# Kernel optimization log

Hardware: AMD Instinct MI355X
Metric: run time of the kernel (lower is better)

The kernel has to match this reference:

```python
import jax, jax.numpy as jnp
import numpy as np

N_HEAD = 16
ROT_DIM = 64  # head_dim * rotary_percentage(1.0)
ROPE_BASE = 10000.0
NEG_INF = -1.0e9


def _rope_cos_sin(seq_len, rd):
    # freqs: [S, rd//2]; original code builds cos/sin per pair; we repeat each
    # entry twice so it applies to the interleaved (even, odd) pair layout.
    inv_freq = 1.0 / (ROPE_BASE ** (jnp.arange(0, rd, 2, dtype=jnp.float32) / rd))
    freqs = jnp.arange(seq_len, dtype=jnp.float32)[:, None] * inv_freq[None, :]
    cos = jnp.repeat(jnp.cos(freqs), 2, axis=-1)  # [S, rd]
    sin = jnp.repeat(jnp.sin(freqs), 2, axis=-1)  # [S, rd]
    return cos, sin


def _rotate_pairs(x):
    # interleaved pairs: (x0, x1) -> (-x1, x0), matching apply_rotary_embeddings
    x2 = x.reshape(x.shape[:-1] + (-1, 2))
    r = jnp.stack([-x2[..., 1], x2[..., 0]], axis=-1)
    return r.reshape(x.shape)


def reference(x, W_attn, W_proj, cache_k, cache_v):
    B, S, D = x.shape
    H = N_HEAD
    HD = D // H
    # fused QKV projection (Linear, bias=False)
    qkv = x @ W_attn  # [B, S, 3D]
    q, k, v = jnp.split(qkv, 3, axis=-1)
    q = q.reshape(B, S, H, HD).transpose(0, 2, 1, 3)  # [B,H,S,HD]
    k = k.reshape(B, S, H, HD).transpose(0, 2, 1, 3)
    v = v.reshape(B, S, H, HD).transpose(0, 2, 1, 3)
    # rotary on first ROT_DIM dims; q = q*cos - rot(q)*sin (original sign conv.)
    cos, sin = _rope_cos_sin(S, ROT_DIM)  # [S, ROT_DIM] broadcasts over B,H
    q_r, q_p = q[..., :ROT_DIM], q[..., ROT_DIM:]
    k_r, k_p = k[..., :ROT_DIM], k[..., ROT_DIM:]
    q_r = q_r * cos - _rotate_pairs(q_r) * sin
    k_r = k_r * cos - _rotate_pairs(k_r) * sin
    q = jnp.concatenate([q_r, q_p], axis=-1)
    k = jnp.concatenate([k_r, k_p], axis=-1)
    # KV-cache write at past_length=0 (prefill), then read back full context
    k_full = jax.lax.dynamic_update_slice(cache_k, k, (0, 0, 0, 0))
    v_full = jax.lax.dynamic_update_slice(cache_v, v, (0, 0, 0, 0))
    T = k_full.shape[2]  # full_seq_len == S here
    # causal additive mask (upper triangular * -1e9), as in the kv_cache branch
    mask = jnp.triu(jnp.ones((T, T), dtype=jnp.float32), k=1) * NEG_INF
    q = q * (1.0 / np.sqrt(HD).astype(np.float32))
    scores = jnp.einsum('bhqd,bhkd->bhqk', q, k_full) + mask
    att = jax.nn.softmax(scores, axis=-1)
    y = jnp.einsum('bhqk,bhkd->bhqd', att, v_full)
    y = y.transpose(0, 2, 1, 3).reshape(B, S, D)
    return y @ W_proj


def setup_inputs() -> dict:
    key = jax.random.key(0)
    k1, k2, k3 = jax.random.split(key, 3)
    B, S, D, H = 2, 2048, 1024, 16
    HD = D // H
    x = jax.random.normal(k1, (B, S, D), dtype=jnp.float32)
    W_attn = jax.random.normal(k2, (D, 3 * D), dtype=jnp.float32) * 0.02
    W_proj = jax.random.normal(k3, (D, D), dtype=jnp.float32) * 0.02
    cache_k = jnp.zeros((B, H, S, HD), dtype=jnp.float32)
    cache_v = jnp.zeros((B, H, S, HD), dtype=jnp.float32)
    return {"x": x, "W_attn": W_attn, "W_proj": W_proj, "cache_k": cache_k, "cache_v": cache_v}
```

## Files before the change

kernel.cpp:

```cpp
#include <hip/hip_runtime.h>
#include <stdint.h>

#define S_LEN 2048
#define NHEAD 16
#define DMODEL 1024

typedef __attribute__((ext_vector_type(8))) short short8;
typedef __attribute__((ext_vector_type(8))) __bf16 bf16x8;
typedef __attribute__((ext_vector_type(4))) float f32x4;
typedef __attribute__((ext_vector_type(16))) float f32x16;

__device__ __forceinline__ unsigned short f2b(float f) {
  unsigned int u = __float_as_uint(f);
  u += 0x7fffu + ((u >> 16) & 1u);
  return (unsigned short)(u >> 16);
}
__device__ __forceinline__ float b2f(unsigned short h) {
  return __uint_as_float(((unsigned int)h) << 16);
}
__device__ __forceinline__ f32x4 mfma16(short8 a, short8 b, f32x4 c) {
  return __builtin_amdgcn_mfma_f32_16x16x32_bf16(
      __builtin_bit_cast(bf16x8, a), __builtin_bit_cast(bf16x8, b), c, 0, 0, 0);
}
__device__ __forceinline__ f32x16 mfma32(short8 a, short8 b, f32x16 c) {
  return __builtin_amdgcn_mfma_f32_32x32x16_bf16(
      __builtin_bit_cast(bf16x8, a), __builtin_bit_cast(bf16x8, b), c, 0, 0, 0);
}
__device__ __forceinline__ unsigned int cvtpk(float lo, float hi) {
  unsigned int r;
  asm("v_cvt_pk_bf16_f32 %0, %1, %2" : "=v"(r) : "v"(lo), "v"(hi));
  return r;
}
__device__ __forceinline__ void gload16(const void* g, void* l) {
  __builtin_amdgcn_global_load_lds(
      (const __attribute__((address_space(1))) unsigned int*)g,
      (__attribute__((address_space(3))) unsigned int*)l, 16, 0, 0);
}

__global__ __launch_bounds__(256) void cast_f32_bf16(
    const float* __restrict__ in, unsigned short* __restrict__ out, long n) {
  long i = ((long)blockIdx.x * 256 + threadIdx.x) * 4;
  if (i >= n) return;
  float4 v = *(const float4*)(in + i);
  ushort4 o;
  o.x = f2b(v.x); o.y = f2b(v.y); o.z = f2b(v.z); o.w = f2b(v.w);
  *(ushort4*)(out + i) = o;
}

__global__ __launch_bounds__(256) void transpose_cast(
    const float* __restrict__ W, unsigned short* __restrict__ Wt, int K, int N) {
  __shared__ float t[32][33];
  const int nt = blockIdx.x, kt = blockIdx.y;
  const int tx = threadIdx.x, ty = threadIdx.y;
#pragma unroll
  for (int j = 0; j < 4; ++j)
    t[ty + j * 8][tx] = W[(long)(kt * 32 + ty + j * 8) * N + nt * 32 + tx];
  __syncthreads();
#pragma unroll
  for (int j = 0; j < 4; ++j)
    Wt[(long)(nt * 32 + ty + j * 8) * K + kt * 32 + tx] = f2b(t[tx][ty + j * 8]);
}

__global__ __launch_bounds__(256) void make_tab(float2* __restrict__ tab) {
  int i = blockIdx.x * 256 + threadIdx.x;
  if (i >= S_LEN * 32) return;
  int s = i >> 5, fi = i & 31;
  float inv = powf(10000.0f, -(float)(2 * fi) / 64.0f);
  float fr = (float)s * inv;
  tab[i] = make_float2(cosf(fr), sinf(fr));
}

template <int OUT_BF16>
__global__ __launch_bounds__(256) void gemm_bt(
    const unsigned short* __restrict__ A, const unsigned short* __restrict__ Bt,
    void* __restrict__ Cout, int M, int N, int K) {
  __shared__ __align__(16) unsigned short As[128 * 32];
  __shared__ __align__(16) unsigned short Bs[128 * 32];
  const int tid = threadIdx.x;
  const int wave = tid >> 6, lane = tid & 63;
  const int g = lane >> 4, r15 = lane & 15;
  const int wm = wave >> 1, wn = wave & 1;
  const long m0 = (long)blockIdx.x * 128, n0 = (long)blockIdx.y * 128;
  const int srow = tid >> 2, scol = (tid & 3) * 8;
  const unsigned short* Ag = A + (m0 + srow) * K + scol;
  const unsigned short* Bg = Bt + (n0 + srow) * K + scol;
  unsigned short* As0 = &As[srow * 32 + scol];
  unsigned short* As1 = &As[(srow + 64) * 32 + scol];
  unsigned short* Bs0 = &Bs[srow * 32 + scol];
  unsigned short* Bs1 = &Bs[(srow + 64) * 32 + scol];
  f32x4 acc[4][4] = {};
  for (int kt = 0; kt < K; kt += 32) {
    __syncthreads();
    gload16(Ag + kt, As0);
    gload16(Ag + (long)64 * K + kt, As1);
    gload16(Bg + kt, Bs0);
    gload16(Bg + (long)64 * K + kt, Bs1);
    __syncthreads();
    short8 a[4], b[4];
#pragma unroll
    for (int m = 0; m < 4; ++m)
      a[m] = *(const short8*)&As[(wm * 64 + m * 16 + r15) * 32 + g * 8];
#pragma unroll
    for (int n = 0; n < 4; ++n)
      b[n] = *(const short8*)&Bs[(wn * 64 + n * 16 + r15) * 32 + g * 8];
#pragma unroll
    for (int m = 0; m < 4; ++m)
#pragma unroll
      for (int n = 0; n < 4; ++n)
        acc[m][n] = mfma16(a[m], b[n], acc[m][n]);
  }
#pragma unroll
  for (int m = 0; m < 4; ++m)
#pragma unroll
    for (int n = 0; n < 4; ++n)
#pragma unroll
      for (int r = 0; r < 4; ++r) {
        long row = m0 + wm * 64 + m * 16 + g * 4 + r;
        long col = n0 + wn * 64 + n * 16 + r15;
        if (OUT_BF16)
          ((unsigned short*)Cout)[row * N + col] = f2b(acc[m][n][r]);
        else
          ((float*)Cout)[row * N + col] = acc[m][n][r];
      }
}

__global__ __launch_bounds__(256) void rope_scatter(
    const unsigned short* __restrict__ qkv, const float2* __restrict__ tab,
    unsigned short* __restrict__ Qb, unsigned short* __restrict__ Kb) {
  long p = (long)blockIdx.x * 256 + threadIdx.x;
  if (p >= (long)4096 * 1024) return;
  int row = (int)(p >> 10);
  int col = ((int)(p & 1023)) * 2;
  int seg = col >> 10;
  int cc = col & 1023;
  int h = cc >> 6, d = cc & 63;
  int b = row >> 11, s = row & 2047;
  const unsigned short* src = qkv + (long)row * 3072 + col;
  float v0 = b2f(src[0]), v1 = b2f(src[1]);
  float2 f = tab[s * 32 + (d >> 1)];
  float o0 = v0 * f.x + v1 * f.y;
  float o1 = v1 * f.x - v0 * f.y;
  float scl = seg ? 1.0f : 0.125f;
  unsigned short* dst = (seg ? Kb : Qb) + (((long)(b * NHEAD + h) * S_LEN + s) * 64 + d);
  dst[0] = f2b(o0 * scl);
  dst[1] = f2b(o1 * scl);
}

__global__ __launch_bounds__(256) void v_transpose(
    const unsigned short* __restrict__ qkv, unsigned short* __restrict__ Vt) {
  __shared__ unsigned short t[64][33];
  const int st = blockIdx.x;
  const int dt = blockIdx.y;
  const int bh = blockIdx.z;
  const int b = bh >> 4, h = bh & 15;
  const int tx = threadIdx.x, ty = threadIdx.y;
#pragma unroll
  for (int j = 0; j < 8; ++j)
    t[ty + j * 8][tx] =
        qkv[((long)b * S_LEN + st * 64 + ty + j * 8) * 3072 + 2048 + h * 64 + dt * 32 + tx];
  __syncthreads();
#pragma unroll
  for (int j = 0; j < 4; ++j) {
    const int d_local = ty + j * 8;
#pragma unroll
    for (int jj = 0; jj < 2; ++jj) {
      const int col = jj * 32 + tx;
      Vt[((long)bh * 64 + dt * 32 + d_local) * S_LEN + st * 64 + col] = t[col][d_local];
    }
  }
}

__device__ __forceinline__ void load_k32(const unsigned short* __restrict__ Kp,
                                         int kv0, int q31, int hi, short8 kf[2][4]) {
#pragma unroll
  for (int sub = 0; sub < 2; ++sub)
#pragma unroll
    for (int dc = 0; dc < 4; ++dc)
      kf[sub][dc] = *(const short8*)(Kp + (long)(kv0 + sub * 32 + q31) * 64 + dc * 16 + hi * 8);
}
__device__ __forceinline__ void load_v32(const unsigned short* __restrict__ Vp,
                                         int kv0, int q31, int hi, short8 vf[2][4]) {
#pragma unroll
  for (int dv = 0; dv < 2; ++dv)
#pragma unroll
    for (int c = 0; c < 4; ++c)
      vf[dv][c] = *(const short8*)(Vp + (long)(dv * 32 + q31) * S_LEN + kv0 + c * 16 + hi * 8);
}

template <bool MASKED, bool PREFETCH>
__device__ __forceinline__ void attn_tile32(
    int kv0, int qbase, int q31, int hi,
    const short8 qf[4], short8 kf[2][4], short8 vf[2][4],
    f32x16& o0, f32x16& o1, float& m, float& l,
    const unsigned short* __restrict__ Kp, const unsigned short* __restrict__ Vp) {
  f32x16 s0 = {}, s1 = {};
#pragma unroll
  for (int dc = 0; dc < 4; ++dc) s0 = mfma32(kf[0][dc], qf[dc], s0);
#pragma unroll
  for (int dc = 0; dc < 4; ++dc) s1 = mfma32(kf[1][dc], qf[dc], s1);
  if (PREFETCH) load_k32(Kp, kv0 + 64, q31, hi, kf);
  if (MASKED) {
    const int q = qbase + q31;
#pragma unroll
    for (int i = 0; i < 16; ++i) {
      const int rel = (i & 3) + 8 * (i >> 2) + 4 * hi;
      s0[i] = (kv0 + rel <= q) ? s0[i] : -1e30f;
      s1[i] = (kv0 + 32 + rel <= q) ? s1[i] : -1e30f;
    }
  }
  float t8[8];
#pragma unroll
  for (int i = 0; i < 8; ++i)
    t8[i] = fmaxf(fmaxf(s0[2 * i], s0[2 * i + 1]), fmaxf(s1[2 * i], s1[2 * i + 1]));
  float mt = fmaxf(fmaxf(fmaxf(t8[0], t8[1]), fmaxf(t8[2], t8[3])),
                   fmaxf(fmaxf(t8[4], t8[5]), fmaxf(t8[6], t8[7])));
  mt = fmaxf(mt, __shfl_xor(mt, 32));
  const float mnew = fmaxf(m, mt);
  const float scl = __expf(m - mnew);
  m = mnew;
#pragma unroll
  for (int i = 0; i < 16; ++i) {
    s0[i] = __expf(s0[i] - mnew);
    s1[i] = __expf(s1[i] - mnew);
  }
  float a8[8];
#pragma unroll
  for (int i = 0; i < 8; ++i)
    a8[i] = (s0[2 * i] + s0[2 * i + 1]) + (s1[2 * i] + s1[2 * i + 1]);
  float rs = ((a8[0] + a8[1]) + (a8[2] + a8[3])) + ((a8[4] + a8[5]) + (a8[6] + a8[7]));
  rs += __shfl_xor(rs, 32);
  l = l * scl + rs;
#pragma unroll
  for (int i = 0; i < 16; ++i) { o0[i] *= scl; o1[i] *= scl; }
#pragma unroll
  for (int c = 0; c < 4; ++c) {
    const int rb = (c & 1) * 8;
    float v0, v1, v2, v3, v4, v5, v6, v7;
    if (c < 2) {
      v0 = s0[rb + 0]; v1 = s0[rb + 1]; v2 = s0[rb + 2]; v3 = s0[rb + 3];
      v4 = s0[rb + 4]; v5 = s0[rb + 5]; v6 = s0[rb + 6]; v7 = s0[rb + 7];
    } else {
      v0 = s1[rb + 0]; v1 = s1[rb + 1]; v2 = s1[rb + 2]; v3 = s1[rb + 3];
      v4 = s1[rb + 4]; v5 = s1[rb + 5]; v6 = s1[rb + 6]; v7 = s1[rb + 7];
    }
    const unsigned int wa = cvtpk(v0, v1), wb = cvtpk(v2, v3);
    const unsigned int wc = cvtpk(v4, v5), wd = cvtpk(v6, v7);
    const unsigned int sa = (unsigned int)__shfl_xor((int)wa, 32);
    const unsigned int sb = (unsigned int)__shfl_xor((int)wb, 32);
    const unsigned int sc_ = (unsigned int)__shfl_xor((int)wc, 32);
    const unsigned int sd = (unsigned int)__shfl_xor((int)wd, 32);
    uint4 pw = hi ? make_uint4(sc_, sd, wc, wd) : make_uint4(wa, wb, sa, sb);
    const short8 pf = __builtin_bit_cast(short8, pw);
    o0 = mfma32(vf[0][c], pf, o0);
    o1 = mfma32(vf[1][c], pf, o1);
  }
  if (PREFETCH) load_v32(Vp, kv0 + 64, q31, hi, vf);
}

__global__ __launch_bounds__(64) void attn_v4(
    const unsigned short* __restrict__ Qb, const unsigned short* __restrict__ Kb,
    const unsigned short* __restrict__ Vt, unsigned short* __restrict__ yb) {
  const int flat = (int)blockIdx.x + ((int)blockIdx.y << 6);
  const int xcd = flat & 7;
  const int rest = flat >> 3;
  const int bh = xcd * 4 + (rest >> 6);
  const int qt = 63 - (rest & 63);
  const int lane = (int)threadIdx.x & 63;
  const int q31 = lane & 31, hi = lane >> 5;
  const int b = bh >> 4, h = bh & 15;
  const int qbase = qt * 32;
  const unsigned short* Kp = Kb + (long)bh * (S_LEN * 64);
  const unsigned short* Vp = Vt + (long)bh * (64 * S_LEN);
  const unsigned short* Qp = Qb + ((long)bh * S_LEN + qbase) * 64;
  short8 qf[4];
#pragma unroll
  for (int dc = 0; dc < 4; ++dc)
    qf[dc] = *(const short8*)(Qp + q31 * 64 + dc * 16 + hi * 8);
  short8 kf[2][4], vf[2][4];
  f32x16 o0 = {}, o1 = {};
  float m = -1e30f, l = 0.f;
  const int nfull = qbase >> 6;

  load_k32(Kp, 0, q31, hi, kf);
  load_v32(Vp, 0, q31, hi, vf);
  for (int t = 0; t < nfull; ++t)
    attn_tile32<false, true>(t * 64, qbase, q31, hi, qf, kf, vf, o0, o1, m, l, Kp, Vp);
  attn_tile32<true, false>(nfull * 64, qbase, q31, hi, qf, kf, vf, o0, o1, m, l, Kp, Vp);

  const float inv = 1.0f / l;
  unsigned short* yrow = yb + ((long)b * S_LEN + qbase + q31) * DMODEL + h * 64;
#pragma unroll
  for (int a2 = 0; a2 < 2; ++a2)
#pragma unroll
    for (int q2 = 0; q2 < 4; ++q2) {
      float e0, e1, e2, e3;
      if (a2 == 0) { e0 = o0[q2 * 4]; e1 = o0[q2 * 4 + 1]; e2 = o0[q2 * 4 + 2]; e3 = o0[q2 * 4 + 3]; }
      else         { e0 = o1[q2 * 4]; e1 = o1[q2 * 4 + 1]; e2 = o1[q2 * 4 + 2]; e3 = o1[q2 * 4 + 3]; }
      uint2 w;
      w.x = cvtpk(e0 * inv, e1 * inv);
      w.y = cvtpk(e2 * inv, e3 * inv);
      *(uint2*)(yrow + a2 * 32 + q2 * 8 + hi * 4) = w;
    }
}

extern "C" void kernel_launch(void* const* d_in, const int* in_sizes, int n_in,
                              void* d_out, int out_size, void* d_ws, size_t ws_size,
                              hipStream_t stream) {
  const float* x = (const float*)d_in[0];
  const float* Wa = (const float*)d_in[1];
  const float* Wp = (const float*)d_in[2];
  float* out = (float*)d_out;

  char* ws = (char*)d_ws;
  size_t off = 0;
  auto alloc = [&](size_t bytes) -> void* {
    off = (off + 255) & ~(size_t)255;
    void* p = ws + off;
    off += bytes;
    return p;
  };
  unsigned short* xb   = (unsigned short*)alloc((size_t)4096 * 1024 * 2);
  unsigned short* WaT  = (unsigned short*)alloc((size_t)3072 * 1024 * 2);
  unsigned short* WpT  = (unsigned short*)alloc((size_t)1024 * 1024 * 2);
  unsigned short* qkvb = (unsigned short*)alloc((size_t)4096 * 3072 * 2);
  float2* tab          = (float2*)alloc((size_t)2048 * 32 * sizeof(float2));
  unsigned short* Qb   = (unsigned short*)alloc((size_t)32 * 2048 * 64 * 2);
  unsigned short* Kb   = (unsigned short*)alloc((size_t)32 * 2048 * 64 * 2);
  unsigned short* Vt   = (unsigned short*)alloc((size_t)32 * 2048 * 64 * 2);
  unsigned short* yb   = xb;

  dim3 tB(32, 8);
  cast_f32_bf16<<<4096, 256, 0, stream>>>(x, xb, (long)4096 * 1024);
  transpose_cast<<<dim3(96, 32), tB, 0, stream>>>(Wa, WaT, 1024, 3072);
  transpose_cast<<<dim3(32, 32), tB, 0, stream>>>(Wp, WpT, 1024, 1024);
  make_tab<<<256, 256, 0, stream>>>(tab);
  gemm_bt<1><<<dim3(32, 24), 256, 0, stream>>>(xb, WaT, (void*)qkvb, 4096, 3072, 1024);
  rope_scatter<<<16384, 256, 0, stream>>>(qkvb, tab, Qb, Kb);
  v_transpose<<<dim3(32, 2, 32), tB, 0, stream>>>(qkvb, Vt);
  attn_v4<<<dim3(64, 32), 64, 0, stream>>>(Qb, Kb, Vt, yb);
  gemm_bt<0><<<dim3(32, 8), 256, 0, stream>>>(yb, WpT, (void*)out, 4096, 1024, 1024);
}
```

Baseline: 277.2 us.

## Split attention KV range across four waves with shared-memory softmax merge

The attention kernel now launches four waves per 32-query tile instead of one. Each wave processes every fourth 64-key tile with its own online softmax state, and the partial outputs and max/sum values are combined through shared memory after a barrier. This targets the long serial KV loop and the causal load imbalance, at the cost of LDS traffic, a synchronisation point and runtime masking branches in place of template specialisation. Waves with no tiles still contribute neutral state (-1e30 max, zero sum).

```diff
diff --git a/kernel.cpp b/kernel.cpp
--- a/kernel.cpp
+++ b/kernel.cpp
@@ -187,9 +187,8 @@
       vf[dv][c] = *(const short8*)(Vp + (long)(dv * 32 + q31) * S_LEN + kv0 + c * 16 + hi * 8);
 }
 
-template <bool MASKED, bool PREFETCH>
 __device__ __forceinline__ void attn_tile32(
-    int kv0, int qbase, int q31, int hi,
+    int kv0, int qbase, int q31, int hi, bool masked, bool pre, int kvn,
     const short8 qf[4], short8 kf[2][4], short8 vf[2][4],
     f32x16& o0, f32x16& o1, float& m, float& l,
     const unsigned short* __restrict__ Kp, const unsigned short* __restrict__ Vp) {
@@ -198,8 +197,8 @@
   for (int dc = 0; dc < 4; ++dc) s0 = mfma32(kf[0][dc], qf[dc], s0);
 #pragma unroll
   for (int dc = 0; dc < 4; ++dc) s1 = mfma32(kf[1][dc], qf[dc], s1);
-  if (PREFETCH) load_k32(Kp, kv0 + 64, q31, hi, kf);
-  if (MASKED) {
+  if (pre) load_k32(Kp, kvn, q31, hi, kf);
+  if (masked) {
     const int q = qbase + q31;
 #pragma unroll
     for (int i = 0; i < 16; ++i) {
@@ -254,18 +253,21 @@
     o0 = mfma32(vf[0][c], pf, o0);
     o1 = mfma32(vf[1][c], pf, o1);
   }
-  if (PREFETCH) load_v32(Vp, kv0 + 64, q31, hi, vf);
-}
-
-__global__ __launch_bounds__(64) void attn_v4(
+  if (pre) load_v32(Vp, kvn, q31, hi, vf);
+}
+
+__global__ __launch_bounds__(256) void attn_v5(
     const unsigned short* __restrict__ Qb, const unsigned short* __restrict__ Kb,
     const unsigned short* __restrict__ Vt, unsigned short* __restrict__ yb) {
+  __shared__ float Om[4][64][33];
+  __shared__ float Ml[4][64][2];
   const int flat = (int)blockIdx.x + ((int)blockIdx.y << 6);
   const int xcd = flat & 7;
   const int rest = flat >> 3;
   const int bh = xcd * 4 + (rest >> 6);
   const int qt = 63 - (rest & 63);
-  const int lane = (int)threadIdx.x & 63;
+  const int tid = (int)threadIdx.x;
+  const int w = tid >> 6, lane = tid & 63;
   const int q31 = lane & 31, hi = lane >> 5;
   const int b = bh >> 4, h = bh & 15;
   const int qbase = qt * 32;
@@ -281,26 +283,50 @@
   float m = -1e30f, l = 0.f;
   const int nfull = qbase >> 6;
 
-  load_k32(Kp, 0, q31, hi, kf);
-  load_v32(Vp, 0, q31, hi, vf);
-  for (int t = 0; t < nfull; ++t)
-    attn_tile32<false, true>(t * 64, qbase, q31, hi, qf, kf, vf, o0, o1, m, l, Kp, Vp);
-  attn_tile32<true, false>(nfull * 64, qbase, q31, hi, qf, kf, vf, o0, o1, m, l, Kp, Vp);
-
-  const float inv = 1.0f / l;
+  if (w <= nfull) {
+    load_k32(Kp, w * 64, q31, hi, kf);
+    load_v32(Vp, w * 64, q31, hi, vf);
+    for (int t = w; t <= nfull; t += 4) {
+      const bool masked = (t == nfull);
+      const bool more = (t + 4 <= nfull);
+      attn_tile32(t * 64, qbase, q31, hi, masked, more, (t + 4) * 64,
+                  qf, kf, vf, o0, o1, m, l, Kp, Vp);
+    }
+  }
+
+  Ml[w][lane][0] = m;
+  Ml[w][lane][1] = l;
+#pragma unroll
+  for (int i = 0; i < 16; ++i) {
+    Om[w][lane][i] = o0[i];
+    Om[w][lane][16 + i] = o1[i];
+  }
+  __syncthreads();
+
+  const float m0 = Ml[0][lane][0], m1 = Ml[1][lane][0];
+  const float m2 = Ml[2][lane][0], m3 = Ml[3][lane][0];
+  const float ms = fmaxf(fmaxf(m0, m1), fmaxf(m2, m3));
+  const float c0 = __expf(m0 - ms), c1 = __expf(m1 - ms);
+  const float c2 = __expf(m2 - ms), c3 = __expf(m3 - ms);
+  const float ls = c0 * Ml[0][lane][1] + c1 * Ml[1][lane][1] +
+                   c2 * Ml[2][lane][1] + c3 * Ml[3][lane][1];
+  const float inv = 1.0f / ls;
   unsigned short* yrow = yb + ((long)b * S_LEN + qbase + q31) * DMODEL + h * 64;
 #pragma unroll
-  for (int a2 = 0; a2 < 2; ++a2)
-#pragma unroll
-    for (int q2 = 0; q2 < 4; ++q2) {
-      float e0, e1, e2, e3;
-      if (a2 == 0) { e0 = o0[q2 * 4]; e1 = o0[q2 * 4 + 1]; e2 = o0[q2 * 4 + 2]; e3 = o0[q2 * 4 + 3]; }
-      else         { e0 = o1[q2 * 4]; e1 = o1[q2 * 4 + 1]; e2 = o1[q2 * 4 + 2]; e3 = o1[q2 * 4 + 3]; }
-      uint2 w;
-      w.x = cvtpk(e0 * inv, e1 * inv);
-      w.y = cvtpk(e2 * inv, e3 * inv);
-      *(uint2*)(yrow + a2 * 32 + q2 * 8 + hi * 4) = w;
-    }
+  for (int k = 0; k < 2; ++k) {
+    const int p8 = w * 2 + k;
+    const int a2 = p8 >> 2, q2 = p8 & 3;
+    const int base = a2 * 16 + q2 * 4;
+    float e[4];
+#pragma unroll
+    for (int j = 0; j < 4; ++j)
+      e[j] = (c0 * Om[0][lane][base + j] + c1 * Om[1][lane][base + j] +
+              c2 * Om[2][lane][base + j] + c3 * Om[3][lane][base + j]) * inv;
+    uint2 wv;
+    wv.x = cvtpk(e[0], e[1]);
+    wv.y = cvtpk(e[2], e[3]);
+    *(uint2*)(yrow + a2 * 32 + q2 * 8 + hi * 4) = wv;
+  }
 }
 
 extern "C" void kernel_launch(void* const* d_in, const int* in_sizes, int n_in,
@@ -337,6 +363,6 @@
   gemm_bt<1><<<dim3(32, 24), 256, 0, stream>>>(xb, WaT, (void*)qkvb, 4096, 3072, 1024);
   rope_scatter<<<16384, 256, 0, stream>>>(qkvb, tab, Qb, Kb);
   v_transpose<<<dim3(32, 2, 32), tB, 0, stream>>>(qkvb, Vt);
-  attn_v4<<<dim3(64, 32), 64, 0, stream>>>(Qb, Kb, Vt, yb);
+  attn_v5<<<dim3(64, 32), 256, 0, stream>>>(Qb, Kb, Vt, yb);
   gemm_bt<0><<<dim3(32, 8), 256, 0, stream>>>(yb, WpT, (void*)out, 4096, 1024, 1024);
 }
```

Measured after the change: 258.4 us. 1.07x faster.
